# Performance work log

Hardware: AMD Instinct MI355X
Metric: run time of the kernel (lower is better)

Reference implementation:

```python
import jax, jax.numpy as jnp
import numpy as np

D_MODEL = 1024
N_HEADS = 16
N_KV_HEADS = 4
D_HEAD = D_MODEL // N_HEADS  # 64
GROUP = N_HEADS // N_KV_HEADS  # 4
SCALE = 1.0 / np.sqrt(D_HEAD)
BATCH, SEQ = 2, 2048


def setup_inputs() -> dict:
    key = jax.random.key(0)
    ks = jax.random.split(key, 12)
    w = 0.02
    qkv = jax.random.normal(ks[0], (BATCH, SEQ, D_MODEL), dtype=jnp.float32)
    # RoPE angles: positions * inverse frequencies, shape [SEQ, D_HEAD//2]
    inv_freq = 1.0 / (10000.0 ** (jnp.arange(0, D_HEAD, 2, dtype=jnp.float32) / D_HEAD))
    pos_emb = jnp.arange(SEQ, dtype=jnp.float32)[:, None] * inv_freq[None, :]
    Wq = jax.random.normal(ks[1], (D_MODEL, D_MODEL), dtype=jnp.float32) * w
    bq = jax.random.normal(ks[2], (D_MODEL,), dtype=jnp.float32) * w
    Wk = jax.random.normal(ks[3], (D_MODEL, N_KV_HEADS * D_HEAD), dtype=jnp.float32) * w
    bk = jax.random.normal(ks[4], (N_KV_HEADS * D_HEAD,), dtype=jnp.float32) * w
    Wv = jax.random.normal(ks[5], (D_MODEL, N_KV_HEADS * D_HEAD), dtype=jnp.float32) * w
    bv = jax.random.normal(ks[6], (N_KV_HEADS * D_HEAD,), dtype=jnp.float32) * w
    Wo = jax.random.normal(ks[7], (D_MODEL, D_MODEL), dtype=jnp.float32) * w
    bo = jax.random.normal(ks[8], (D_MODEL,), dtype=jnp.float32) * w
    return {"qkv": qkv, "pos_emb": pos_emb, "Wq": Wq, "bq": bq, "Wk": Wk, "bk": bk,
            "Wv": Wv, "bv": bv, "Wo": Wo, "bo": bo}


def _rotate_half(x):
    x1, x2 = jnp.split(x, 2, axis=-1)
    return jnp.concatenate([-x2, x1], axis=-1)


def _apply_rope(q, k, pos_emb):
    # q: [B,S,H,Dh], k: [B,S,Kv,Dh], pos_emb: [S, Dh/2] angles
    cos = jnp.cos(pos_emb)
    sin = jnp.sin(pos_emb)
    cos = jnp.concatenate([cos, cos], axis=-1)[None, :, None, :]  # [1,S,1,Dh]
    sin = jnp.concatenate([sin, sin], axis=-1)[None, :, None, :]
    q = q * cos + _rotate_half(q) * sin
    k = k * cos + _rotate_half(k) * sin
    return q, k


def reference(qkv, pos_emb, Wq, bq, Wk, bk, Wv, bv, Wo, bo):
    B, S, D = qkv.shape
    q = qkv @ Wq + bq                           # [B,S,D]
    k = qkv @ Wk + bk                           # [B,S,Kv*Dh]
    v = qkv @ Wv + bv
    q = q.reshape(B, S, N_HEADS, D_HEAD)
    k = k.reshape(B, S, N_KV_HEADS, D_HEAD)
    v = v.reshape(B, S, N_KV_HEADS, D_HEAD)
    q, k = _apply_rope(q, k, pos_emb)
    q = q.transpose(0, 2, 1, 3)                 # [B,H,S,Dh]
    k = k.transpose(0, 2, 1, 3)                 # [B,Kv,S,Dh]
    v = v.transpose(0, 2, 1, 3)
    # GQA: replicate each kv head across its query-head group
    k = jnp.repeat(k, GROUP, axis=1)            # [B,H,S,Dh]
    v = jnp.repeat(v, GROUP, axis=1)
    scores = jnp.einsum('bhqd,bhkd->bhqk', q, k) * SCALE
    causal = jnp.tril(jnp.ones((S, S), dtype=bool))
    scores = jnp.where(causal[None, None, :, :], scores, jnp.finfo(scores.dtype).min)
    attn = jax.nn.softmax(scores, axis=-1)
    out = jnp.einsum('bhqk,bhkd->bhqd', attn, v)  # [B,H,S,Dh]
    out = out.transpose(0, 2, 1, 3).reshape(B, S, D)
    return out @ Wo + bo
```

## Files before the change

### kernel.cpp

```cpp
#include <hip/hip_runtime.h>
#include <hip/hip_bf16.h>

using f32x4  = __attribute__((ext_vector_type(4))) float;
using short8 = __attribute__((ext_vector_type(8))) short;
using u16    = unsigned short;
using u32    = unsigned int;

#define B_SZ   2
#define S_LEN  2048
#define NH     16
#define NKV    4
#define DH     64
#define DM     1024
#define NQKVC  1536
#define MROWS  4096
#define QSCALE 0.18033688011112042f

__device__ __forceinline__ u16 f2bf(float f) {
  return __builtin_bit_cast(u16, __float2bfloat16(f));
}
__device__ __forceinline__ float bf2f(u16 b) {
  return __builtin_bit_cast(float, ((u32)b) << 16);
}
__device__ __forceinline__ void gld16(const void* g, void* l) {
  __builtin_amdgcn_global_load_lds((const __attribute__((address_space(1))) u32*)g,
                                   (__attribute__((address_space(3))) u32*)l, 16, 0, 0);
}

__global__ void k_cast_x(const float* __restrict__ x, u16* __restrict__ xb) {
  int i = (blockIdx.x * 256 + threadIdx.x) * 4;
  float4 v = *(const float4*)(x + i);
  ushort4 o;
  o.x = f2bf(v.x); o.y = f2bf(v.y); o.z = f2bf(v.z); o.w = f2bf(v.w);
  *(ushort4*)(xb + i) = o;
}

__global__ void k_transpose_w(const float* __restrict__ w, int ncols, u16* __restrict__ wt) {
  __shared__ float t[32][33];
  int k0 = blockIdx.x * 32, n0 = blockIdx.y * 32;
  int tx = threadIdx.x, ty = threadIdx.y;
#pragma unroll
  for (int j = 0; j < 32; j += 8)
    t[ty + j][tx] = w[(size_t)(k0 + ty + j) * ncols + n0 + tx];
  __syncthreads();
#pragma unroll
  for (int j = 0; j < 32; j += 8)
    wt[(size_t)(n0 + ty + j) * 1024 + k0 + tx] = f2bf(t[tx][ty + j]);
}

__global__ void k_prep_small(const float* __restrict__ bq, const float* __restrict__ bk,
                             const float* __restrict__ bv, const float* __restrict__ pe,
                             float* __restrict__ biasqkv, float* __restrict__ cs,
                             float* __restrict__ sn) {
  int i = blockIdx.x * 256 + threadIdx.x;
  if (i < NQKVC)
    biasqkv[i] = (i < 1024) ? bq[i] : (i < 1280 ? bk[i - 1024] : bv[i - 1280]);
  if (i < S_LEN * 32) {
    float a = pe[i];
    cs[i] = cosf(a);
    sn[i] = sinf(a);
  }
}

template <typename OUT_T>
__global__ __launch_bounds__(256) void k_gemm(const u16* __restrict__ A,
                                              const u16* __restrict__ Bt,
                                              const float* __restrict__ bias,
                                              OUT_T* __restrict__ C,
                                              int M, int N, int K) {
  __shared__ u16 la[128 * 32];
  __shared__ u16 lb[128 * 32];
  const int tid = threadIdx.x;
  const int m0 = blockIdx.x * 128, n0 = blockIdx.y * 128;
  const int lane = tid & 63, wv = tid >> 6;
  const int g = lane >> 4, lr = lane & 15;
  const int wr = wv >> 1, wc = wv & 1;

  const int srow0 = (wv * 2 + 0) * 16 + (lane >> 2);
  const int srow1 = (wv * 2 + 1) * 16 + (lane >> 2);
  const int scol = (lane & 3) * 8;
  const u16* pa0 = A  + (size_t)(m0 + srow0) * K + scol;
  const u16* pa1 = A  + (size_t)(m0 + srow1) * K + scol;
  const u16* pb0 = Bt + (size_t)(n0 + srow0) * K + scol;
  const u16* pb1 = Bt + (size_t)(n0 + srow1) * K + scol;
  u16* lda0 = &la[(wv * 2 + 0) * 512];
  u16* lda1 = &la[(wv * 2 + 1) * 512];
  u16* ldb0 = &lb[(wv * 2 + 0) * 512];
  u16* ldb1 = &lb[(wv * 2 + 1) * 512];

  f32x4 acc[4][4] = {};
  const int nk = K >> 5;
  for (int kt = 0; kt < nk; ++kt) {
    const int ko = kt * 32;
    gld16(pa0 + ko, lda0);
    gld16(pa1 + ko, lda1);
    gld16(pb0 + ko, ldb0);
    gld16(pb1 + ko, ldb1);
    __syncthreads();
    short8 af[4], bfr[4];
#pragma unroll
    for (int m = 0; m < 4; ++m)
      af[m] = *(const short8*)&la[(64 * wr + 16 * m + lr) * 32 + 8 * g];
#pragma unroll
    for (int n = 0; n < 4; ++n)
      bfr[n] = *(const short8*)&lb[(64 * wc + 16 * n + lr) * 32 + 8 * g];
#pragma unroll
    for (int m = 0; m < 4; ++m)
#pragma unroll
      for (int n = 0; n < 4; ++n)
        acc[m][n] = __builtin_amdgcn_mfma_f32_16x16x32_bf16(af[m], bfr[n], acc[m][n], 0, 0, 0);
    __syncthreads();
  }

#pragma unroll
  for (int m = 0; m < 4; ++m)
#pragma unroll
    for (int n = 0; n < 4; ++n) {
      const int col = n0 + 64 * wc + 16 * n + lr;
      const float bz = bias[col];
#pragma unroll
      for (int r = 0; r < 4; ++r) {
        const int row = m0 + 64 * wr + 16 * m + 4 * g + r;
        float v = acc[m][n][r] + bz;
        if constexpr (sizeof(OUT_T) == 2) C[(size_t)row * N + col] = f2bf(v);
        else                              C[(size_t)row * N + col] = v;
      }
    }
}

__global__ void k_rope_qk(const u16* __restrict__ p, const float* __restrict__ cs,
                          const float* __restrict__ sn, u16* __restrict__ Qr,
                          u16* __restrict__ Kr) {
  const int row = blockIdx.x;
  const int b = row >> 11, s = row & 2047;
  const u16* pr = p + (size_t)row * NQKVC;
  const float* crow = cs + s * 32;
  const float* srow = sn + s * 32;
  const int tid = threadIdx.x;
#pragma unroll
  for (int it = 0; it < 4; ++it) {
    int c = it * 256 + tid;
    int h = c >> 6, d = c & 63, j = d & 31;
    float x = bf2f(pr[c]);
    float y = bf2f(pr[c ^ 32]);
    float o = (x * crow[j] + (d < 32 ? -y : y) * srow[j]) * QSCALE;
    Qr[((size_t)(b * NH + h) * S_LEN + s) * DH + d] = f2bf(o);
  }
  {
    int c = 1024 + tid;
    int kvh = tid >> 6, d = tid & 63, j = d & 31;
    float x = bf2f(pr[c]);
    float y = bf2f(pr[c ^ 32]);
    float o = x * crow[j] + (d < 32 ? -y : y) * srow[j];
    Kr[((size_t)(b * NKV + kvh) * S_LEN + s) * DH + d] = f2bf(o);
  }
}

__global__ void k_vpack(const u16* __restrict__ p, u16* __restrict__ Vt) {
  __shared__ u16 t[32][33];
  const int st = blockIdx.x * 32;
  const int dt = blockIdx.y * 32;
  const int bkv = blockIdx.z;
  const int b = bkv >> 2, kv = bkv & 3;
  const int tx = threadIdx.x, ty = threadIdx.y;
#pragma unroll
  for (int j = 0; j < 32; j += 8)
    t[ty + j][tx] = p[(size_t)(b * S_LEN + st + ty + j) * NQKVC + 1280 + kv * 64 + dt + tx];
  __syncthreads();
#pragma unroll
  for (int j = 0; j < 32; j += 8)
    Vt[((size_t)(b * NKV + kv) * DH + dt + ty + j) * S_LEN + st + tx] = t[tx][ty + j];
}

__global__ __launch_bounds__(256, 2) void k_attn(const u16* __restrict__ Qr,
                                                 const u16* __restrict__ Kr,
                                                 const u16* __restrict__ Vt,
                                                 u16* __restrict__ Og) {
  __shared__ u16 kbuf[2][4096];
  __shared__ u16 vbuf[2][4096];
  __shared__ u16 plds[4][16][72];

  const int tid = threadIdx.x, wv = tid >> 6, lane = tid & 63;
  const int g = lane >> 4, lr = lane & 15;
  const int wg = blockIdx.x;
  const int xcd = wg & 7, iw = wg >> 3;
  const int bh = xcd * 4 + (iw & 3);
  const int pr = iw >> 2;
  const int b = bh >> 4, h = bh & 15, kv = h >> 2;

  const u16* Kbase = Kr + (size_t)(b * NKV + kv) * S_LEN * DH;
  const u16* Vbase = Vt + (size_t)(b * NKV + kv) * DH * S_LEN;

  const int sr = tid >> 3;
  const int sc = tid & 7;
  const int ssw = sc ^ (sr & 7);
  const int rsw = lr & 7;
  u16* prow = &plds[wv][lr][0];

  for (int pass = 0; pass < 2; ++pass) {
    const int qt = pass ? (31 - pr) : pr;
    const int Q0 = qt * 64;
    const int q0w = Q0 + wv * 16;
    const int myq = q0w + lr;

    const u16* Qb = Qr + ((size_t)(b * NH + h) * S_LEN + q0w) * DH;
    short8 qf0 = *(const short8*)(Qb + lr * DH + 8 * g);
    short8 qf1 = *(const short8*)(Qb + lr * DH + 32 + 8 * g);

    float m = -1e30f, l = 0.f;
    f32x4 accO[4] = {};
    const f32x4 z = {};

    const int nt = qt + 1;
    {
      gld16(Kbase + (size_t)sr * DH + ssw * 8,        &kbuf[0][wv * 512]);
      gld16(Kbase + (size_t)(sr + 32) * DH + ssw * 8, &kbuf[0][2048 + wv * 512]);
      gld16(Vbase + (size_t)sr * S_LEN + ssw * 8,        &vbuf[0][wv * 512]);
      gld16(Vbase + (size_t)(sr + 32) * S_LEN + ssw * 8, &vbuf[0][2048 + wv * 512]);
    }
    __syncthreads();
    int buf = 0;
    for (int ti = 0; ti < nt; ++ti) {
      const int kb = ti * 64;
      if (ti + 1 < nt) {
        const int kn = kb + 64;
        gld16(Kbase + (size_t)(kn + sr) * DH + ssw * 8,      &kbuf[buf ^ 1][wv * 512]);
        gld16(Kbase + (size_t)(kn + sr + 32) * DH + ssw * 8, &kbuf[buf ^ 1][2048 + wv * 512]);
        gld16(Vbase + (size_t)sr * S_LEN + kn + ssw * 8,        &vbuf[buf ^ 1][wv * 512]);
        gld16(Vbase + (size_t)(sr + 32) * S_LEN + kn + ssw * 8, &vbuf[buf ^ 1][2048 + wv * 512]);
      }
      const u16* kl = kbuf[buf];
      const u16* vl = vbuf[buf];
      short8 k0[4], k1[4];
#pragma unroll
      for (int t = 0; t < 4; ++t) {
        const int row = 16 * t + lr;
        k0[t] = *(const short8*)&kl[row * 64 + (g ^ rsw) * 8];
        k1[t] = *(const short8*)&kl[row * 64 + ((4 + g) ^ rsw) * 8];
      }
      f32x4 s[4];
      __builtin_amdgcn_s_setprio(1);
#pragma unroll
      for (int t = 0; t < 4; ++t) {
        s[t] = __builtin_amdgcn_mfma_f32_16x16x32_bf16(k0[t], qf0, z, 0, 0, 0);
        s[t] = __builtin_amdgcn_mfma_f32_16x16x32_bf16(k1[t], qf1, s[t], 0, 0, 0);
      }
      __builtin_amdgcn_s_setprio(0);
      if (kb + 63 > q0w) {
#pragma unroll
        for (int t = 0; t < 4; ++t)
#pragma unroll
          for (int r = 0; r < 4; ++r)
            if (kb + 16 * t + 4 * g + r > myq) s[t][r] = -1e30f;
      }
      float a0 = fmaxf(fmaxf(s[0][0], s[0][1]), fmaxf(s[0][2], s[0][3]));
      float a1 = fmaxf(fmaxf(s[1][0], s[1][1]), fmaxf(s[1][2], s[1][3]));
      float a2 = fmaxf(fmaxf(s[2][0], s[2][1]), fmaxf(s[2][2], s[2][3]));
      float a3 = fmaxf(fmaxf(s[3][0], s[3][1]), fmaxf(s[3][2], s[3][3]));
      float tm = fmaxf(fmaxf(a0, a1), fmaxf(a2, a3));
      tm = fmaxf(tm, __shfl_xor(tm, 16));
      tm = fmaxf(tm, __shfl_xor(tm, 32));
      if (__any(tm > m + 8.f)) {
        float mn = fmaxf(tm, m);
        float al = __builtin_exp2f(m - mn);
        m = mn;
        l *= al;
#pragma unroll
        for (int t = 0; t < 4; ++t) {
          accO[t][0] *= al; accO[t][1] *= al; accO[t][2] *= al; accO[t][3] *= al;
        }
      }
      float rs = 0.f;
#pragma unroll
      for (int t = 0; t < 4; ++t)
#pragma unroll
        for (int r = 0; r < 4; ++r) {
          float e = __builtin_exp2f(s[t][r] - m);
          s[t][r] = e;
          rs += e;
        }
      rs += __shfl_xor(rs, 16);
      rs += __shfl_xor(rs, 32);
      l += rs;
#pragma unroll
      for (int t = 0; t < 4; ++t) {
        u32 lo = (u32)f2bf(s[t][0]) | ((u32)f2bf(s[t][1]) << 16);
        u32 hi = (u32)f2bf(s[t][2]) | ((u32)f2bf(s[t][3]) << 16);
        uint2 w2; w2.x = lo; w2.y = hi;
        *(uint2*)(prow + 16 * t + 4 * g) = w2;
      }
      short8 pb0 = *(const short8*)(prow + 8 * g);
      short8 pb1 = *(const short8*)(prow + 32 + 8 * g);
      __builtin_amdgcn_s_setprio(1);
#pragma unroll
      for (int t = 0; t < 4; ++t) {
        const int row = 16 * t + lr;
        short8 vf0 = *(const short8*)&vl[row * 64 + (g ^ rsw) * 8];
        short8 vf1 = *(const short8*)&vl[row * 64 + ((4 + g) ^ rsw) * 8];
        accO[t] = __builtin_amdgcn_mfma_f32_16x16x32_bf16(vf0, pb0, accO[t], 0, 0, 0);
        accO[t] = __builtin_amdgcn_mfma_f32_16x16x32_bf16(vf1, pb1, accO[t], 0, 0, 0);
      }
      __builtin_amdgcn_s_setprio(0);
      __syncthreads();
      buf ^= 1;
    }

    const float inv = 1.0f / l;
    u16* orow = Og + ((size_t)(b * S_LEN + q0w + lr)) * DM + h * DH;
#pragma unroll
    for (int t = 0; t < 4; ++t) {
      ushort4 o;
      o.x = f2bf(accO[t][0] * inv);
      o.y = f2bf(accO[t][1] * inv);
      o.z = f2bf(accO[t][2] * inv);
      o.w = f2bf(accO[t][3] * inv);
      *(ushort4*)(orow + 16 * t + 4 * g) = o;
    }
    __syncthreads();
  }
}

extern "C" void kernel_launch(void* const* d_in, const int* in_sizes, int n_in,
                              void* d_out, int out_size, void* d_ws, size_t ws_size,
                              hipStream_t stream) {
  const float* x  = (const float*)d_in[0];
  const float* pe = (const float*)d_in[1];
  const float* Wq = (const float*)d_in[2];
  const float* bq = (const float*)d_in[3];
  const float* Wk = (const float*)d_in[4];
  const float* bk = (const float*)d_in[5];
  const float* Wv = (const float*)d_in[6];
  const float* bv = (const float*)d_in[7];
  const float* Wo = (const float*)d_in[8];
  const float* bo = (const float*)d_in[9];
  float* out = (float*)d_out;

  char* w = (char*)d_ws;
  u16* Xb      = (u16*)w;   w += (size_t)MROWS * DM * 2;
  u16* Wqkvt   = (u16*)w;   w += (size_t)NQKVC * DM * 2;
  u16* Wot     = (u16*)w;   w += (size_t)DM * DM * 2;
  float* biasq = (float*)w; w += NQKVC * 4;
  float* cs    = (float*)w; w += S_LEN * 32 * 4;
  float* sn    = (float*)w; w += S_LEN * 32 * 4;
  u16* QKVp    = (u16*)w;   w += (size_t)MROWS * NQKVC * 2;
  u16* Qr      = (u16*)w;   w += (size_t)B_SZ * NH * S_LEN * DH * 2;
  u16* Kr      = (u16*)w;   w += (size_t)B_SZ * NKV * S_LEN * DH * 2;
  u16* Vt      = (u16*)w;   w += (size_t)B_SZ * NKV * DH * S_LEN * 2;
  u16* Og      = (u16*)w;

  dim3 tb(32, 8);
  k_cast_x<<<MROWS * DM / (256 * 4), 256, 0, stream>>>(x, Xb);
  k_transpose_w<<<dim3(32, 32), tb, 0, stream>>>(Wq, 1024, Wqkvt);
  k_transpose_w<<<dim3(32, 8),  tb, 0, stream>>>(Wk, 256,  Wqkvt + (size_t)1024 * 1024);
  k_transpose_w<<<dim3(32, 8),  tb, 0, stream>>>(Wv, 256,  Wqkvt + (size_t)1280 * 1024);
  k_transpose_w<<<dim3(32, 32), tb, 0, stream>>>(Wo, 1024, Wot);
  k_prep_small<<<(S_LEN * 32 + 255) / 256, 256, 0, stream>>>(bq, bk, bv, pe, biasq, cs, sn);

  k_gemm<u16><<<dim3(MROWS / 128, NQKVC / 128), 256, 0, stream>>>(
      Xb, Wqkvt, biasq, QKVp, MROWS, NQKVC, DM);

  k_rope_qk<<<MROWS, 256, 0, stream>>>(QKVp, cs, sn, Qr, Kr);
  k_vpack<<<dim3(S_LEN / 32, DH / 32, B_SZ * NKV), tb, 0, stream>>>(QKVp, Vt);

  k_attn<<<512, 256, 0, stream>>>(Qr, Kr, Vt, Og);

  k_gemm<float><<<dim3(MROWS / 128, DM / 128), 256, 0, stream>>>(
      Og, Wot, bo, out, MROWS, DM, DM);
}
```

Measured before the change: 214.5 us.

## Merge prep and rope/vpack launches, shrink GEMM N tile, run both attention query tiles concurrently

```diff
diff --git a/kernel.cpp b/kernel.cpp
--- a/kernel.cpp
+++ b/kernel.cpp
@@ -27,18 +27,11 @@
                                    (__attribute__((address_space(3))) u32*)l, 16, 0, 0);
 }
 
-__global__ void k_cast_x(const float* __restrict__ x, u16* __restrict__ xb) {
-  int i = (blockIdx.x * 256 + threadIdx.x) * 4;
-  float4 v = *(const float4*)(x + i);
-  ushort4 o;
-  o.x = f2bf(v.x); o.y = f2bf(v.y); o.z = f2bf(v.z); o.w = f2bf(v.w);
-  *(ushort4*)(xb + i) = o;
-}
-
-__global__ void k_transpose_w(const float* __restrict__ w, int ncols, u16* __restrict__ wt) {
-  __shared__ float t[32][33];
-  int k0 = blockIdx.x * 32, n0 = blockIdx.y * 32;
-  int tx = threadIdx.x, ty = threadIdx.y;
+__device__ __forceinline__ void transp_tile(const float* __restrict__ w, int ncols,
+                                            u16* __restrict__ wt, int bx, int by,
+                                            int tid, float (*t)[33]) {
+  const int k0 = bx * 32, n0 = by * 32;
+  const int tx = tid & 31, ty = tid >> 5;
 #pragma unroll
   for (int j = 0; j < 32; j += 8)
     t[ty + j][tx] = w[(size_t)(k0 + ty + j) * ncols + n0 + tx];
@@ -48,14 +41,41 @@
     wt[(size_t)(n0 + ty + j) * 1024 + k0 + tx] = f2bf(t[tx][ty + j]);
 }
 
-__global__ void k_prep_small(const float* __restrict__ bq, const float* __restrict__ bk,
-                             const float* __restrict__ bv, const float* __restrict__ pe,
-                             float* __restrict__ biasqkv, float* __restrict__ cs,
-                             float* __restrict__ sn) {
-  int i = blockIdx.x * 256 + threadIdx.x;
-  if (i < NQKVC)
-    biasqkv[i] = (i < 1024) ? bq[i] : (i < 1280 ? bk[i - 1024] : bv[i - 1280]);
-  if (i < S_LEN * 32) {
+__global__ __launch_bounds__(256) void k_prep(
+    const float* __restrict__ x, u16* __restrict__ xb,
+    const float* __restrict__ Wq, const float* __restrict__ Wk,
+    const float* __restrict__ Wv, const float* __restrict__ Wo,
+    u16* __restrict__ Wqkvt, u16* __restrict__ Wot,
+    const float* __restrict__ bq, const float* __restrict__ bk,
+    const float* __restrict__ bv, const float* __restrict__ pe,
+    float* __restrict__ biasqkv, float* __restrict__ cs, float* __restrict__ sn) {
+  __shared__ float tt[32][33];
+  const int job = blockIdx.x, tid = threadIdx.x;
+  if (job < 1024) {
+#pragma unroll
+    for (int u = 0; u < 4; ++u) {
+      int i = job * 4096 + u * 1024 + tid * 4;
+      float4 v = *(const float4*)(x + i);
+      ushort4 o;
+      o.x = f2bf(v.x); o.y = f2bf(v.y); o.z = f2bf(v.z); o.w = f2bf(v.w);
+      *(ushort4*)(xb + i) = o;
+    }
+  } else if (job < 2048) {
+    int t = job - 1024;
+    transp_tile(Wq, 1024, Wqkvt, t & 31, t >> 5, tid, tt);
+  } else if (job < 2304) {
+    int t = job - 2048;
+    transp_tile(Wk, 256, Wqkvt + (size_t)1024 * 1024, t & 31, t >> 5, tid, tt);
+  } else if (job < 2560) {
+    int t = job - 2304;
+    transp_tile(Wv, 256, Wqkvt + (size_t)1280 * 1024, t & 31, t >> 5, tid, tt);
+  } else if (job < 3584) {
+    int t = job - 2560;
+    transp_tile(Wo, 1024, Wot, t & 31, t >> 5, tid, tt);
+  } else {
+    int i = (job - 3584) * 256 + tid;
+    if (i < NQKVC)
+      biasqkv[i] = (i < 1024) ? bq[i] : (i < 1280 ? bk[i - 1024] : bv[i - 1280]);
     float a = pe[i];
     cs[i] = cosf(a);
     sn[i] = sinf(a);
@@ -69,45 +89,41 @@
                                               OUT_T* __restrict__ C,
                                               int M, int N, int K) {
   __shared__ u16 la[128 * 32];
-  __shared__ u16 lb[128 * 32];
+  __shared__ u16 lb[64 * 32];
   const int tid = threadIdx.x;
-  const int m0 = blockIdx.x * 128, n0 = blockIdx.y * 128;
+  const int m0 = blockIdx.x * 128, n0 = blockIdx.y * 64;
   const int lane = tid & 63, wv = tid >> 6;
   const int g = lane >> 4, lr = lane & 15;
   const int wr = wv >> 1, wc = wv & 1;
 
-  const int srow0 = (wv * 2 + 0) * 16 + (lane >> 2);
-  const int srow1 = (wv * 2 + 1) * 16 + (lane >> 2);
-  const int scol = (lane & 3) * 8;
-  const u16* pa0 = A  + (size_t)(m0 + srow0) * K + scol;
-  const u16* pa1 = A  + (size_t)(m0 + srow1) * K + scol;
-  const u16* pb0 = Bt + (size_t)(n0 + srow0) * K + scol;
-  const u16* pb1 = Bt + (size_t)(n0 + srow1) * K + scol;
-  u16* lda0 = &la[(wv * 2 + 0) * 512];
-  u16* lda1 = &la[(wv * 2 + 1) * 512];
-  u16* ldb0 = &lb[(wv * 2 + 0) * 512];
-  u16* ldb1 = &lb[(wv * 2 + 1) * 512];
-
-  f32x4 acc[4][4] = {};
+  const int sr = tid >> 2;
+  const int scol = (tid & 3) * 8;
+  const u16* pa0 = A  + (size_t)(m0 + sr) * K + scol;
+  const u16* pa1 = A  + (size_t)(m0 + 64 + sr) * K + scol;
+  const u16* pb  = Bt + (size_t)(n0 + sr) * K + scol;
+  u16* lda0 = &la[wv * 512];
+  u16* lda1 = &la[2048 + wv * 512];
+  u16* ldb  = &lb[wv * 512];
+
+  f32x4 acc[4][2] = {};
   const int nk = K >> 5;
   for (int kt = 0; kt < nk; ++kt) {
     const int ko = kt * 32;
     gld16(pa0 + ko, lda0);
     gld16(pa1 + ko, lda1);
-    gld16(pb0 + ko, ldb0);
-    gld16(pb1 + ko, ldb1);
+    gld16(pb + ko, ldb);
     __syncthreads();
-    short8 af[4], bfr[4];
+    short8 af[4], bfr[2];
 #pragma unroll
     for (int m = 0; m < 4; ++m)
       af[m] = *(const short8*)&la[(64 * wr + 16 * m + lr) * 32 + 8 * g];
 #pragma unroll
-    for (int n = 0; n < 4; ++n)
-      bfr[n] = *(const short8*)&lb[(64 * wc + 16 * n + lr) * 32 + 8 * g];
+    for (int n = 0; n < 2; ++n)
+      bfr[n] = *(const short8*)&lb[(32 * wc + 16 * n + lr) * 32 + 8 * g];
 #pragma unroll
     for (int m = 0; m < 4; ++m)
 #pragma unroll
-      for (int n = 0; n < 4; ++n)
+      for (int n = 0; n < 2; ++n)
         acc[m][n] = __builtin_amdgcn_mfma_f32_16x16x32_bf16(af[m], bfr[n], acc[m][n], 0, 0, 0);
     __syncthreads();
   }
@@ -115,8 +131,8 @@
 #pragma unroll
   for (int m = 0; m < 4; ++m)
 #pragma unroll
-    for (int n = 0; n < 4; ++n) {
-      const int col = n0 + 64 * wc + 16 * n + lr;
+    for (int n = 0; n < 2; ++n) {
+      const int col = n0 + 32 * wc + 16 * n + lr;
       const float bz = bias[col];
 #pragma unroll
       for (int r = 0; r < 4; ++r) {
@@ -128,65 +144,74 @@
     }
 }
 
-__global__ void k_rope_qk(const u16* __restrict__ p, const float* __restrict__ cs,
-                          const float* __restrict__ sn, u16* __restrict__ Qr,
-                          u16* __restrict__ Kr) {
-  const int row = blockIdx.x;
-  const int b = row >> 11, s = row & 2047;
-  const u16* pr = p + (size_t)row * NQKVC;
-  const float* crow = cs + s * 32;
-  const float* srow = sn + s * 32;
-  const int tid = threadIdx.x;
-#pragma unroll
-  for (int it = 0; it < 4; ++it) {
-    int c = it * 256 + tid;
-    int h = c >> 6, d = c & 63, j = d & 31;
-    float x = bf2f(pr[c]);
-    float y = bf2f(pr[c ^ 32]);
-    float o = (x * crow[j] + (d < 32 ? -y : y) * srow[j]) * QSCALE;
-    Qr[((size_t)(b * NH + h) * S_LEN + s) * DH + d] = f2bf(o);
-  }
-  {
-    int c = 1024 + tid;
-    int kvh = tid >> 6, d = tid & 63, j = d & 31;
-    float x = bf2f(pr[c]);
-    float y = bf2f(pr[c ^ 32]);
-    float o = x * crow[j] + (d < 32 ? -y : y) * srow[j];
-    Kr[((size_t)(b * NKV + kvh) * S_LEN + s) * DH + d] = f2bf(o);
-  }
-}
-
-__global__ void k_vpack(const u16* __restrict__ p, u16* __restrict__ Vt) {
-  __shared__ u16 t[32][33];
-  const int st = blockIdx.x * 32;
-  const int dt = blockIdx.y * 32;
-  const int bkv = blockIdx.z;
-  const int b = bkv >> 2, kv = bkv & 3;
-  const int tx = threadIdx.x, ty = threadIdx.y;
-#pragma unroll
-  for (int j = 0; j < 32; j += 8)
-    t[ty + j][tx] = p[(size_t)(b * S_LEN + st + ty + j) * NQKVC + 1280 + kv * 64 + dt + tx];
-  __syncthreads();
-#pragma unroll
-  for (int j = 0; j < 32; j += 8)
-    Vt[((size_t)(b * NKV + kv) * DH + dt + ty + j) * S_LEN + st + tx] = t[tx][ty + j];
-}
-
-__global__ __launch_bounds__(256, 2) void k_attn(const u16* __restrict__ Qr,
+__global__ __launch_bounds__(256) void k_rv(const u16* __restrict__ p,
+                                            const float* __restrict__ cs,
+                                            const float* __restrict__ sn,
+                                            u16* __restrict__ Qr, u16* __restrict__ Kr,
+                                            u16* __restrict__ Vt) {
+  __shared__ u16 tt[32][33];
+  const int job = blockIdx.x, tid = threadIdx.x;
+  if (job < 4096) {
+    const int row = job;
+    const int b = row >> 11, s = row & 2047;
+    const u16* pr = p + (size_t)row * NQKVC;
+    const float* crow = cs + s * 32;
+    const float* srow = sn + s * 32;
+#pragma unroll
+    for (int it = 0; it < 4; ++it) {
+      int c = it * 256 + tid;
+      int h = c >> 6, d = c & 63, j = d & 31;
+      float x = bf2f(pr[c]);
+      float y = bf2f(pr[c ^ 32]);
+      float o = (x * crow[j] + (d < 32 ? -y : y) * srow[j]) * QSCALE;
+      Qr[((size_t)(b * NH + h) * S_LEN + s) * DH + d] = f2bf(o);
+    }
+    {
+      int c = 1024 + tid;
+      int kvh = tid >> 6, d = tid & 63, j = d & 31;
+      float x = bf2f(pr[c]);
+      float y = bf2f(pr[c ^ 32]);
+      float o = x * crow[j] + (d < 32 ? -y : y) * srow[j];
+      Kr[((size_t)(b * NKV + kvh) * S_LEN + s) * DH + d] = f2bf(o);
+    }
+  } else {
+    const int idx = job - 4096;
+    const int st = (idx & 63) * 32;
+    const int dt = ((idx >> 6) & 1) * 32;
+    const int bkv = idx >> 7;
+    const int b = bkv >> 2, kv = bkv & 3;
+    const int tx = tid & 31, ty = tid >> 5;
+#pragma unroll
+    for (int j = 0; j < 32; j += 8)
+      tt[ty + j][tx] = p[(size_t)(b * S_LEN + st + ty + j) * NQKVC + 1280 + kv * 64 + dt + tx];
+    __syncthreads();
+#pragma unroll
+    for (int j = 0; j < 32; j += 8)
+      Vt[((size_t)(b * NKV + kv) * DH + dt + ty + j) * S_LEN + st + tx] = tt[tx][ty + j];
+  }
+}
+
+__global__ __launch_bounds__(512, 4) void k_attn(const u16* __restrict__ Qr,
                                                  const u16* __restrict__ Kr,
                                                  const u16* __restrict__ Vt,
                                                  u16* __restrict__ Og) {
   __shared__ u16 kbuf[2][4096];
   __shared__ u16 vbuf[2][4096];
-  __shared__ u16 plds[4][16][72];
+  __shared__ u16 plds[8][16][72];
 
   const int tid = threadIdx.x, wv = tid >> 6, lane = tid & 63;
   const int g = lane >> 4, lr = lane & 15;
   const int wg = blockIdx.x;
   const int xcd = wg & 7, iw = wg >> 3;
   const int bh = xcd * 4 + (iw & 3);
-  const int pr = iw >> 2;
+  const int j = iw >> 2;
+  const int pr = (j < 8) ? j : 23 - j;
   const int b = bh >> 4, h = bh & 15, kv = h >> 2;
+  const int qt = (wv >> 2) ? (31 - pr) : pr;
+  const int q0w = qt * 64 + (wv & 3) * 16;
+  const int myq = q0w + lr;
+  const int myNt = qt + 1;
+  const int nt = 32 - pr;
 
   const u16* Kbase = Kr + (size_t)(b * NKV + kv) * S_LEN * DH;
   const u16* Vbase = Vt + (size_t)(b * NKV + kv) * DH * S_LEN;
@@ -197,38 +222,26 @@
   const int rsw = lr & 7;
   u16* prow = &plds[wv][lr][0];
 
-  for (int pass = 0; pass < 2; ++pass) {
-    const int qt = pass ? (31 - pr) : pr;
-    const int Q0 = qt * 64;
-    const int q0w = Q0 + wv * 16;
-    const int myq = q0w + lr;
-
-    const u16* Qb = Qr + ((size_t)(b * NH + h) * S_LEN + q0w) * DH;
-    short8 qf0 = *(const short8*)(Qb + lr * DH + 8 * g);
-    short8 qf1 = *(const short8*)(Qb + lr * DH + 32 + 8 * g);
-
-    float m = -1e30f, l = 0.f;
-    f32x4 accO[4] = {};
-    const f32x4 z = {};
-
-    const int nt = qt + 1;
-    {
-      gld16(Kbase + (size_t)sr * DH + ssw * 8,        &kbuf[0][wv * 512]);
-      gld16(Kbase + (size_t)(sr + 32) * DH + ssw * 8, &kbuf[0][2048 + wv * 512]);
-      gld16(Vbase + (size_t)sr * S_LEN + ssw * 8,        &vbuf[0][wv * 512]);
-      gld16(Vbase + (size_t)(sr + 32) * S_LEN + ssw * 8, &vbuf[0][2048 + wv * 512]);
-    }
-    __syncthreads();
-    int buf = 0;
-    for (int ti = 0; ti < nt; ++ti) {
-      const int kb = ti * 64;
-      if (ti + 1 < nt) {
-        const int kn = kb + 64;
-        gld16(Kbase + (size_t)(kn + sr) * DH + ssw * 8,      &kbuf[buf ^ 1][wv * 512]);
-        gld16(Kbase + (size_t)(kn + sr + 32) * DH + ssw * 8, &kbuf[buf ^ 1][2048 + wv * 512]);
-        gld16(Vbase + (size_t)sr * S_LEN + kn + ssw * 8,        &vbuf[buf ^ 1][wv * 512]);
-        gld16(Vbase + (size_t)(sr + 32) * S_LEN + kn + ssw * 8, &vbuf[buf ^ 1][2048 + wv * 512]);
-      }
+  const u16* Qb = Qr + ((size_t)(b * NH + h) * S_LEN + q0w) * DH;
+  short8 qf0 = *(const short8*)(Qb + lr * DH + 8 * g);
+  short8 qf1 = *(const short8*)(Qb + lr * DH + 32 + 8 * g);
+
+  float m = -1e30f, l = 0.f;
+  f32x4 accO[4] = {};
+  const f32x4 z = {};
+
+  gld16(Kbase + (size_t)sr * DH + ssw * 8,    &kbuf[0][wv * 512]);
+  gld16(Vbase + (size_t)sr * S_LEN + ssw * 8, &vbuf[0][wv * 512]);
+  __syncthreads();
+  int buf = 0;
+  for (int ti = 0; ti < nt; ++ti) {
+    const int kb = ti * 64;
+    if (ti + 1 < nt) {
+      const int kn = kb + 64;
+      gld16(Kbase + (size_t)(kn + sr) * DH + ssw * 8,   &kbuf[buf ^ 1][wv * 512]);
+      gld16(Vbase + (size_t)sr * S_LEN + kn + ssw * 8,  &vbuf[buf ^ 1][wv * 512]);
+    }
+    if (ti < myNt) {
       const u16* kl = kbuf[buf];
       const u16* vl = vbuf[buf];
       short8 k0[4], k1[4];
@@ -253,10 +266,10 @@
           for (int r = 0; r < 4; ++r)
             if (kb + 16 * t + 4 * g + r > myq) s[t][r] = -1e30f;
       }
-      float a0 = fmaxf(fmaxf(s[0][0], s[0][1]), fmaxf(s[0][2], s[0][3]));
-      float a1 = fmaxf(fmaxf(s[1][0], s[1][1]), fmaxf(s[1][2], s[1][3]));
-      float a2 = fmaxf(fmaxf(s[2][0], s[2][1]), fmaxf(s[2][2], s[2][3]));
-      float a3 = fmaxf(fmaxf(s[3][0], s[3][1]), fmaxf(s[3][2], s[3][3]));
+      float a0 = fmaxf(fmaxf(fmaxf(s[0][0], s[0][1]), s[0][2]), s[0][3]);
+      float a1 = fmaxf(fmaxf(fmaxf(s[1][0], s[1][1]), s[1][2]), s[1][3]);
+      float a2 = fmaxf(fmaxf(fmaxf(s[2][0], s[2][1]), s[2][2]), s[2][3]);
+      float a3 = fmaxf(fmaxf(fmaxf(s[3][0], s[3][1]), s[3][2]), s[3][3]);
       float tm = fmaxf(fmaxf(a0, a1), fmaxf(a2, a3));
       tm = fmaxf(tm, __shfl_xor(tm, 16));
       tm = fmaxf(tm, __shfl_xor(tm, 32));
@@ -301,22 +314,21 @@
         accO[t] = __builtin_amdgcn_mfma_f32_16x16x32_bf16(vf1, pb1, accO[t], 0, 0, 0);
       }
       __builtin_amdgcn_s_setprio(0);
-      __syncthreads();
-      buf ^= 1;
-    }
-
-    const float inv = 1.0f / l;
-    u16* orow = Og + ((size_t)(b * S_LEN + q0w + lr)) * DM + h * DH;
-#pragma unroll
-    for (int t = 0; t < 4; ++t) {
-      ushort4 o;
-      o.x = f2bf(accO[t][0] * inv);
-      o.y = f2bf(accO[t][1] * inv);
-      o.z = f2bf(accO[t][2] * inv);
-      o.w = f2bf(accO[t][3] * inv);
-      *(ushort4*)(orow + 16 * t + 4 * g) = o;
     }
     __syncthreads();
+    buf ^= 1;
+  }
+
+  const float inv = 1.0f / l;
+  u16* orow = Og + ((size_t)(b * S_LEN + q0w + lr)) * DM + h * DH;
+#pragma unroll
+  for (int t = 0; t < 4; ++t) {
+    ushort4 o;
+    o.x = f2bf(accO[t][0] * inv);
+    o.y = f2bf(accO[t][1] * inv);
+    o.z = f2bf(accO[t][2] * inv);
+    o.w = f2bf(accO[t][3] * inv);
+    *(ushort4*)(orow + 16 * t + 4 * g) = o;
   }
 }
 
@@ -348,22 +360,16 @@
   u16* Vt      = (u16*)w;   w += (size_t)B_SZ * NKV * DH * S_LEN * 2;
   u16* Og      = (u16*)w;
 
-  dim3 tb(32, 8);
-  k_cast_x<<<MROWS * DM / (256 * 4), 256, 0, stream>>>(x, Xb);
-  k_transpose_w<<<dim3(32, 32), tb, 0, stream>>>(Wq, 1024, Wqkvt);
-  k_transpose_w<<<dim3(32, 8),  tb, 0, stream>>>(Wk, 256,  Wqkvt + (size_t)1024 * 1024);
-  k_transpose_w<<<dim3(32, 8),  tb, 0, stream>>>(Wv, 256,  Wqkvt + (size_t)1280 * 1024);
-  k_transpose_w<<<dim3(32, 32), tb, 0, stream>>>(Wo, 1024, Wot);
-  k_prep_small<<<(S_LEN * 32 + 255) / 256, 256, 0, stream>>>(bq, bk, bv, pe, biasq, cs, sn);
-
-  k_gemm<u16><<<dim3(MROWS / 128, NQKVC / 128), 256, 0, stream>>>(
+  k_prep<<<3840, 256, 0, stream>>>(x, Xb, Wq, Wk, Wv, Wo, Wqkvt, Wot,
+                                   bq, bk, bv, pe, biasq, cs, sn);
+
+  k_gemm<u16><<<dim3(MROWS / 128, NQKVC / 64), 256, 0, stream>>>(
       Xb, Wqkvt, biasq, QKVp, MROWS, NQKVC, DM);
 
-  k_rope_qk<<<MROWS, 256, 0, stream>>>(QKVp, cs, sn, Qr, Kr);
-  k_vpack<<<dim3(S_LEN / 32, DH / 32, B_SZ * NKV), tb, 0, stream>>>(QKVp, Vt);
-
-  k_attn<<<512, 256, 0, stream>>>(Qr, Kr, Vt, Og);
-
-  k_gemm<float><<<dim3(MROWS / 128, DM / 128), 256, 0, stream>>>(
+  k_rv<<<4096 + 1024, 256, 0, stream>>>(QKVp, cs, sn, Qr, Kr, Vt);
+
+  k_attn<<<512, 512, 0, stream>>>(Qr, Kr, Vt, Og);
+
+  k_gemm<float><<<dim3(MROWS / 128, DM / 64), 256, 0, stream>>>(
       Og, Wot, bo, out, MROWS, DM, DM);
 }
```

Result: faster. 187.2 us (-12.7%).
